# Kernel tuning notes

Hardware: AMD Instinct MI355X
Metric: run time of the kernel (lower is better)

## Reference

```python
import jax, jax.numpy as jnp
import numpy as np

N = 100000
E = 1600000
IN_DIM, HID, OUT = 128, 64, 16
NUM_CLASSES = 2
BN_EPS = 1e-5


def setup_inputs() -> dict:
    key = jax.random.key(0)
    ks = jax.random.split(key, 12)
    s = lambda fan_in: 1.0 / np.sqrt(fan_in)
    inp = {
        'x': jax.random.normal(ks[0], (N, IN_DIM), jnp.float32),
        'src': jax.random.randint(ks[1], (E,), 0, N, jnp.int32),
        'dst': jax.random.randint(ks[2], (E,), 0, N, jnp.int32),
        # SAGEConv1: lin_l (neighbors, bias) + lin_r (root, no bias)
        'W1l': jax.random.uniform(ks[3], (HID, IN_DIM), jnp.float32, -s(IN_DIM), s(IN_DIM)),
        'b1l': jnp.zeros((HID,), jnp.float32),
        'W1r': jax.random.uniform(ks[4], (HID, IN_DIM), jnp.float32, -s(IN_DIM), s(IN_DIM)),
        # BatchNorm1d(hidden)
        'gamma': jnp.ones((HID,), jnp.float32),
        'beta': jnp.zeros((HID,), jnp.float32),
        # SAGEConv2
        'W2l': jax.random.uniform(ks[5], (OUT, HID), jnp.float32, -s(HID), s(HID)),
        'b2l': jnp.zeros((OUT,), jnp.float32),
        'W2r': jax.random.uniform(ks[6], (OUT, HID), jnp.float32, -s(HID), s(HID)),
        # classifier Linear(emb_dim=16, 2)
        'Wc': jax.random.uniform(ks[7], (NUM_CLASSES, OUT), jnp.float32, -s(OUT), s(OUT)),
        'bc': jax.random.uniform(ks[8], (NUM_CLASSES,), jnp.float32, -s(OUT), s(OUT)),
    }
    return inp


def _sage_conv(x, src, dst, Wl, bl, Wr, deg_inv):
    # mean-aggregate neighbor features at dst, then linear; plus root transform
    agg = jax.ops.segment_sum(x[src], dst, num_segments=N) * deg_inv  # [N, F]
    return agg @ Wl.T + bl + x @ Wr.T


def _batchnorm_train(h, gamma, beta):
    mu = jnp.mean(h, axis=0)
    var = jnp.mean((h - mu) ** 2, axis=0)  # biased, as torch BN uses for normalization
    return (h - mu) * jax.lax.rsqrt(var + BN_EPS) * gamma + beta


def reference(x, src, dst, W1l, b1l, W1r, gamma, beta, W2l, b2l, W2r, Wc, bc):
    deg = jax.ops.segment_sum(jnp.ones((E,), x.dtype), dst, num_segments=N)
    deg_inv = (1.0 / jnp.maximum(deg, 1.0))[:, None]
    h = _sage_conv(x, src, dst, W1l, b1l, W1r, deg_inv)      # [N, HID]
    h = jax.nn.relu(_batchnorm_train(h, gamma, beta))
    emb = _sage_conv(h, src, dst, W2l, b2l, W2r, deg_inv)    # [N, OUT]
    logits = emb @ Wc.T + bc                                 # [N, 2]
    return (logits, emb)
```

## Files before the change

### kernel.cpp

```cpp
#include <hip/hip_runtime.h>

#define NN 100000
#define NB ((NN + 255) / 256)

__device__ __forceinline__ void gemm32x64(const float* __restrict__ x,
        const float* __restrict__ W, float* __restrict__ out,
        int rb, int tid, float (*lw)[68], float (*lx)[68]) {
    const int row0 = rb * 32;
    const int cg = tid & 15, rl = tid >> 4;
    float acc[2][4] = {{0.f,0.f,0.f,0.f},{0.f,0.f,0.f,0.f}};
    for (int kt = 0; kt < 2; ++kt) {
        if (kt) __syncthreads();
        for (int idx = tid; idx < 4096; idx += 256) {
            int j = idx >> 6, k = idx & 63;
            lw[k][j] = W[j * 128 + kt * 64 + k];
        }
        #pragma unroll
        for (int i = 0; i < 2; ++i) {
            int f4 = i * 256 + tid;
            int r = f4 >> 4, k4 = (f4 & 15) << 2;
            int grow = row0 + r;
            float4 vv = make_float4(0.f, 0.f, 0.f, 0.f);
            if (grow < NN) vv = *(const float4*)(x + (size_t)grow * 128 + kt * 64 + k4);
            *(float4*)(&lx[r][k4]) = vv;
        }
        __syncthreads();
        #pragma unroll
        for (int p = 0; p < 2; ++p) {
            int r = p * 16 + rl;
            #pragma unroll 8
            for (int k = 0; k < 64; ++k) {
                float xv = lx[r][k];
                float4 wv = *(const float4*)(&lw[k][cg << 2]);
                acc[p][0] = fmaf(xv, wv.x, acc[p][0]);
                acc[p][1] = fmaf(xv, wv.y, acc[p][1]);
                acc[p][2] = fmaf(xv, wv.z, acc[p][2]);
                acc[p][3] = fmaf(xv, wv.w, acc[p][3]);
            }
        }
    }
    #pragma unroll
    for (int p = 0; p < 2; ++p) {
        int grow = row0 + p * 16 + rl;
        if (grow < NN)
            *(float4*)(out + (size_t)grow * 64 + (cg << 2)) =
                make_float4(acc[p][0], acc[p][1], acc[p][2], acc[p][3]);
    }
}

__global__ __launch_bounds__(256) void k_fusedA(const float* __restrict__ x,
        const float* __restrict__ W1l, const int* __restrict__ dst,
        int* __restrict__ deg, float* __restrict__ y1, int E) {
    __shared__ float lw[64][68];
    __shared__ float lx[32][68];
    const int tid = threadIdx.x;
    const int u = blockIdx.x >> 4, v = blockIdx.x & 15;
    if (v < 8) {
        const int base = (u * 8 + v) * 512;
        #pragma unroll
        for (int i = 0; i < 2; ++i) {
            int e = base + i * 256 + tid;
            if (e < E) atomicAdd(&deg[dst[e]], 1);
        }
        return;
    }
    const int rb = u * 8 + (v - 8);
    if (rb >= 3125) return;
    gemm32x64(x, W1l, y1, rb, tid, lw, lx);
}

__global__ __launch_bounds__(256) void k_fusedB(const float* __restrict__ x,
        const float* __restrict__ W1r, const int* __restrict__ src,
        const int* __restrict__ dst, int* __restrict__ cursor,
        int* __restrict__ eidx, float* __restrict__ h, int E) {
    __shared__ float lw[64][68];
    __shared__ float lx[32][68];
    const int tid = threadIdx.x;
    const int u = blockIdx.x >> 4, v = blockIdx.x & 15;
    if (v < 8) {
        const int base = u * 4096;
        const int lo = v * 12500, hi = lo + 12500;
        #pragma unroll 4
        for (int i = 0; i < 16; ++i) {
            int e = base + i * 256 + tid;
            if (e < E) {
                int d = dst[e];
                if (d >= lo && d < hi) {
                    int pos = atomicAdd(&cursor[d], 1);
                    eidx[pos] = src[e];
                }
            }
        }
        return;
    }
    const int rb = u * 8 + (v - 8);
    if (rb >= 3125) return;
    gemm32x64(x, W1r, h, rb, tid, lw, lx);
}

__global__ __launch_bounds__(256) void k_scanA(const int* __restrict__ deg,
                                               int* __restrict__ rowptr,
                                               int* __restrict__ bsum) {
    const int tid = threadIdx.x;
    const int i = blockIdx.x * 256 + tid;
    int v = (i < NN) ? deg[i] : 0;
    const int lane = tid & 63, w = tid >> 6;
    int inc = v;
    #pragma unroll
    for (int d = 1; d < 64; d <<= 1) {
        int t = __shfl_up(inc, d, 64);
        if (lane >= d) inc += t;
    }
    __shared__ int wsum[4];
    if (lane == 63) wsum[w] = inc;
    __syncthreads();
    int wo = 0;
    for (int k = 0; k < w; ++k) wo += wsum[k];
    if (i < NN) rowptr[i] = wo + inc - v;
    if (tid == 255) bsum[blockIdx.x] = wo + inc;
}

__global__ __launch_bounds__(512) void k_scanB(int* __restrict__ bsum,
                                               int* __restrict__ rowptr, int E) {
    const int tid = threadIdx.x;
    int v = (tid < NB) ? bsum[tid] : 0;
    const int lane = tid & 63, w = tid >> 6;
    int inc = v;
    #pragma unroll
    for (int d = 1; d < 64; d <<= 1) {
        int t = __shfl_up(inc, d, 64);
        if (lane >= d) inc += t;
    }
    __shared__ int wsum[8];
    if (lane == 63) wsum[w] = inc;
    __syncthreads();
    int wo = 0;
    for (int k = 0; k < w; ++k) wo += wsum[k];
    if (tid < NB) bsum[tid] = wo + inc - v;
    if (tid == 0) rowptr[NN] = E;
}

__global__ void k_finish(int* __restrict__ rowptr, const int* __restrict__ bsum,
                         const int* __restrict__ deg, int* __restrict__ cursor,
                         float* __restrict__ deg_inv) {
    int i = blockIdx.x * 256 + threadIdx.x;
    if (i < NN) {
        int rp = rowptr[i] + bsum[i >> 8];
        rowptr[i] = rp;
        cursor[i] = rp;
        deg_inv[i] = 1.0f / fmaxf((float)deg[i], 1.0f);
    }
}

__global__ __launch_bounds__(256) void k_gather1(const float* __restrict__ y1,
        const int* __restrict__ rowptr, const int* __restrict__ eidx,
        const float* __restrict__ b1l,
        const float* __restrict__ deg_inv, float* __restrict__ h,
        float* __restrict__ stats) {
    const int tid = threadIdx.x;
    const int f = tid & 63, w = tid >> 6;
    const float bias = b1l[f];
    float a1 = 0.f, a2 = 0.f;
    for (int n = blockIdx.x * 4 + w; n < NN; n += gridDim.x * 4) {
        int beg = rowptr[n], end = rowptr[n + 1];
        float s0 = 0.f, s1 = 0.f, s2 = 0.f, s3 = 0.f;
        int j = beg;
        for (; j + 3 < end; j += 4) {
            int i0 = eidx[j], i1 = eidx[j + 1], i2 = eidx[j + 2], i3 = eidx[j + 3];
            s0 += y1[(size_t)i0 * 64 + f];
            s1 += y1[(size_t)i1 * 64 + f];
            s2 += y1[(size_t)i2 * 64 + f];
            s3 += y1[(size_t)i3 * 64 + f];
        }
        for (; j < end; ++j) s0 += y1[(size_t)eidx[j] * 64 + f];
        size_t off = (size_t)n * 64 + f;
        float hv = fmaf((s0 + s1) + (s2 + s3), deg_inv[n], h[off] + bias);
        h[off] = hv;
        a1 += hv; a2 = fmaf(hv, hv, a2);
    }
    __shared__ float sA[4][64], sB[4][64];
    sA[w][f] = a1; sB[w][f] = a2;
    __syncthreads();
    if (w == 0) {
        atomicAdd(&stats[f],      sA[0][f] + sA[1][f] + sA[2][f] + sA[3][f]);
        atomicAdd(&stats[64 + f], sB[0][f] + sB[1][f] + sB[2][f] + sB[3][f]);
    }
}

__global__ void k_bn_final(float* __restrict__ stats, const float* __restrict__ gamma,
                           const float* __restrict__ beta) {
    int f = threadIdx.x;
    float mu = stats[f] * (1.0f / NN);
    float var = stats[64 + f] * (1.0f / NN) - mu * mu;
    float sc = gamma[f] * rsqrtf(var + 1e-5f);
    stats[128 + f] = sc;
    stats[192 + f] = beta[f] - mu * sc;
}

__global__ __launch_bounds__(256) void k_gemm2(const float* __restrict__ h,
        const float* __restrict__ W2l, const float* __restrict__ W2r,
        const float* __restrict__ stats,
        float* __restrict__ y2, float* __restrict__ hr2) {
    __shared__ float lh[64][68];
    __shared__ float lw[64][36];
    const int tid = threadIdx.x;
    for (int idx = tid; idx < 32 * 64; idx += 256) {
        int j = idx >> 6, k = idx & 63;
        lw[k][j] = (j < 16) ? W2l[idx] : W2r[idx - 1024];
    }
    const int row0 = blockIdx.x * 64;
    for (int i = 0; i < 4; ++i) {
        int f4 = i * 256 + tid;
        int r = f4 >> 4;
        int k4 = (f4 & 15) << 2;
        int grow = row0 + r;
        float4 v = make_float4(0.f, 0.f, 0.f, 0.f);
        if (grow < NN) v = *(const float4*)(h + (size_t)grow * 64 + k4);
        float4 sc = *(const float4*)(stats + 128 + k4);
        float4 sh = *(const float4*)(stats + 192 + k4);
        float4 o;
        o.x = fmaxf(fmaf(v.x, sc.x, sh.x), 0.f);
        o.y = fmaxf(fmaf(v.y, sc.y, sh.y), 0.f);
        o.z = fmaxf(fmaf(v.z, sc.z, sh.z), 0.f);
        o.w = fmaxf(fmaf(v.w, sc.w, sh.w), 0.f);
        *(float4*)(&lh[r][k4]) = o;
    }
    __syncthreads();
    const int cg = tid & 7;
    const int rl = tid >> 3;
    #pragma unroll
    for (int p = 0; p < 2; ++p) {
        int r = p * 32 + rl;
        int grow = row0 + r;
        float ax = 0.f, ay = 0.f, az = 0.f, aw = 0.f;
        #pragma unroll
        for (int k = 0; k < 64; ++k) {
            float hv = lh[r][k];
            float4 wv = *(const float4*)(&lw[k][cg << 2]);
            ax = fmaf(hv, wv.x, ax); ay = fmaf(hv, wv.y, ay);
            az = fmaf(hv, wv.z, az); aw = fmaf(hv, wv.w, aw);
        }
        if (grow < NN) {
            int c = cg << 2;
            if (c < 16) *(float4*)(y2  + (size_t)grow * 16 + c)        = make_float4(ax, ay, az, aw);
            else        *(float4*)(hr2 + (size_t)grow * 16 + (c - 16)) = make_float4(ax, ay, az, aw);
        }
    }
}

__global__ __launch_bounds__(256) void k_gather2(const float* __restrict__ y2,
        const int* __restrict__ rowptr, const int* __restrict__ eidx,
        const float* __restrict__ hr2, const float* __restrict__ b2l,
        const float* __restrict__ deg_inv, const float* __restrict__ Wc,
        const float* __restrict__ bc, float* __restrict__ out) {
    const int tid = threadIdx.x;
    const int f = tid & 15, g = tid >> 4;
    const float wc0 = Wc[f], wc1 = Wc[16 + f];
    const float bias = b2l[f];
    for (int n = blockIdx.x * 16 + g; n < NN; n += gridDim.x * 16) {
        int beg = rowptr[n], end = rowptr[n + 1];
        float s0 = 0.f, s1 = 0.f, s2 = 0.f, s3 = 0.f;
        int j = beg;
        for (; j + 3 < end; j += 4) {
            int i0 = eidx[j], i1 = eidx[j + 1], i2 = eidx[j + 2], i3 = eidx[j + 3];
            s0 += y2[(size_t)i0 * 16 + f];
            s1 += y2[(size_t)i1 * 16 + f];
            s2 += y2[(size_t)i2 * 16 + f];
            s3 += y2[(size_t)i3 * 16 + f];
        }
        for (; j < end; ++j) s0 += y2[(size_t)eidx[j] * 16 + f];
        float e = fmaf((s0 + s1) + (s2 + s3), deg_inv[n], hr2[(size_t)n * 16 + f] + bias);
        out[(size_t)(2 * NN) + (size_t)n * 16 + f] = e;
        float l0 = e * wc0, l1 = e * wc1;
        #pragma unroll
        for (int m = 1; m < 16; m <<= 1) {
            l0 += __shfl_xor(l0, m, 64);
            l1 += __shfl_xor(l1, m, 64);
        }
        if (f == 0) {
            out[(size_t)n * 2]     = l0 + bc[0];
            out[(size_t)n * 2 + 1] = l1 + bc[1];
        }
    }
}

extern "C" void kernel_launch(void* const* d_in, const int* in_sizes, int n_in,
                              void* d_out, int out_size, void* d_ws, size_t ws_size,
                              hipStream_t stream) {
    const float* x     = (const float*)d_in[0];
    const int*   src   = (const int*)d_in[1];
    const int*   dst   = (const int*)d_in[2];
    const float* W1l   = (const float*)d_in[3];
    const float* b1l   = (const float*)d_in[4];
    const float* W1r   = (const float*)d_in[5];
    const float* gamma = (const float*)d_in[6];
    const float* beta  = (const float*)d_in[7];
    const float* W2l   = (const float*)d_in[8];
    const float* b2l   = (const float*)d_in[9];
    const float* W2r   = (const float*)d_in[10];
    const float* Wc    = (const float*)d_in[11];
    const float* bc    = (const float*)d_in[12];
    const int E = in_sizes[1];

    float* ws      = (float*)d_ws;
    int*   rowptr  = (int*)ws;
    float* deg_inv = ws + 100352;
    float* stats   = ws + 200704;
    int*   deg_i   = (int*)(ws + 200960);
    int*   cursor  = (int*)(ws + 301312);
    int*   eidx    = (int*)(ws + 401664);
    float* y1      = ws + 401664 + (size_t)E;
    float* h       = y1 + (size_t)NN * 64;
    int*   bsum    = eidx;
    float* y2      = y1;
    float* hr2     = y1 + (size_t)NN * 16;
    float* out     = (float*)d_out;

    hipMemsetAsync(deg_i, 0, NN * sizeof(int), stream);
    hipMemsetAsync(stats, 0, 256 * sizeof(float), stream);

    k_fusedA<<<6256, 256, 0, stream>>>(x, W1l, dst, deg_i, y1, E);

    k_scanA<<<NB, 256, 0, stream>>>(deg_i, rowptr, bsum);
    k_scanB<<<1, 512, 0, stream>>>(bsum, rowptr, E);
    k_finish<<<NB, 256, 0, stream>>>(rowptr, bsum, deg_i, cursor, deg_inv);

    k_fusedB<<<6256, 256, 0, stream>>>(x, W1r, src, dst, cursor, eidx, h, E);

    k_gather1<<<4096, 256, 0, stream>>>(y1, rowptr, eidx, b1l, deg_inv, h, stats);
    k_bn_final<<<1, 64, 0, stream>>>(stats, gamma, beta);

    k_gemm2<<<(NN + 63) / 64, 256, 0, stream>>>(h, W2l, W2r, stats, y2, hr2);

    k_gather2<<<2048, 256, 0, stream>>>(y2, rowptr, eidx, hr2, b2l, deg_inv, Wc, bc, out);
}
```

Before: 473.8 us.

## Store gathered neighbor features in bf16 and fold BN finalize into gemm2

The per-node transformed features y1 and y2, which are gathered once per edge, are now stored as bf16 instead of fp32. This halves the bytes moved in the two edge gathers. Separately, the tiny BN-finalize kernel is removed and each gemm2 block computes the scale and shift itself into shared memory, saving one launch. The cost is reduced precision in the aggregated messages, which may shift the outputs relative to the fp32 reference.

```diff
diff --git a/kernel.cpp b/kernel.cpp
--- a/kernel.cpp
+++ b/kernel.cpp
@@ -3,8 +3,18 @@
 #define NN 100000
 #define NB ((NN + 255) / 256)
 
+__device__ __forceinline__ unsigned short f2bf(float x) {
+    unsigned u = __float_as_uint(x);
+    u += 0x7fff + ((u >> 16) & 1);
+    return (unsigned short)(u >> 16);
+}
+__device__ __forceinline__ float bf2f(unsigned short h) {
+    return __uint_as_float(((unsigned)h) << 16);
+}
+
+template<bool BF16>
 __device__ __forceinline__ void gemm32x64(const float* __restrict__ x,
-        const float* __restrict__ W, float* __restrict__ out,
+        const float* __restrict__ W, void* __restrict__ out,
         int rb, int tid, float (*lw)[68], float (*lx)[68]) {
     const int row0 = rb * 32;
     const int cg = tid & 15, rl = tid >> 4;
@@ -42,15 +52,23 @@
     #pragma unroll
     for (int p = 0; p < 2; ++p) {
         int grow = row0 + p * 16 + rl;
-        if (grow < NN)
-            *(float4*)(out + (size_t)grow * 64 + (cg << 2)) =
-                make_float4(acc[p][0], acc[p][1], acc[p][2], acc[p][3]);
+        if (grow < NN) {
+            if (BF16) {
+                ushort4 o;
+                o.x = f2bf(acc[p][0]); o.y = f2bf(acc[p][1]);
+                o.z = f2bf(acc[p][2]); o.w = f2bf(acc[p][3]);
+                *(ushort4*)((unsigned short*)out + (size_t)grow * 64 + (cg << 2)) = o;
+            } else {
+                *(float4*)((float*)out + (size_t)grow * 64 + (cg << 2)) =
+                    make_float4(acc[p][0], acc[p][1], acc[p][2], acc[p][3]);
+            }
+        }
     }
 }
 
 __global__ __launch_bounds__(256) void k_fusedA(const float* __restrict__ x,
         const float* __restrict__ W1l, const int* __restrict__ dst,
-        int* __restrict__ deg, float* __restrict__ y1, int E) {
+        int* __restrict__ deg, unsigned short* __restrict__ y1, int E) {
     __shared__ float lw[64][68];
     __shared__ float lx[32][68];
     const int tid = threadIdx.x;
@@ -66,7 +84,7 @@
     }
     const int rb = u * 8 + (v - 8);
     if (rb >= 3125) return;
-    gemm32x64(x, W1l, y1, rb, tid, lw, lx);
+    gemm32x64<true>(x, W1l, y1, rb, tid, lw, lx);
 }
 
 __global__ __launch_bounds__(256) void k_fusedB(const float* __restrict__ x,
@@ -95,7 +113,7 @@
     }
     const int rb = u * 8 + (v - 8);
     if (rb >= 3125) return;
-    gemm32x64(x, W1r, h, rb, tid, lw, lx);
+    gemm32x64<false>(x, W1r, h, rb, tid, lw, lx);
 }
 
 __global__ __launch_bounds__(256) void k_scanA(const int* __restrict__ deg,
@@ -152,7 +170,7 @@
     }
 }
 
-__global__ __launch_bounds__(256) void k_gather1(const float* __restrict__ y1,
+__global__ __launch_bounds__(256) void k_gather1(const unsigned short* __restrict__ y1,
         const int* __restrict__ rowptr, const int* __restrict__ eidx,
         const float* __restrict__ b1l,
         const float* __restrict__ deg_inv, float* __restrict__ h,
@@ -167,12 +185,12 @@
         int j = beg;
         for (; j + 3 < end; j += 4) {
             int i0 = eidx[j], i1 = eidx[j + 1], i2 = eidx[j + 2], i3 = eidx[j + 3];
-            s0 += y1[(size_t)i0 * 64 + f];
-            s1 += y1[(size_t)i1 * 64 + f];
-            s2 += y1[(size_t)i2 * 64 + f];
-            s3 += y1[(size_t)i3 * 64 + f];
-        }
-        for (; j < end; ++j) s0 += y1[(size_t)eidx[j] * 64 + f];
+            s0 += bf2f(y1[(size_t)i0 * 64 + f]);
+            s1 += bf2f(y1[(size_t)i1 * 64 + f]);
+            s2 += bf2f(y1[(size_t)i2 * 64 + f]);
+            s3 += bf2f(y1[(size_t)i3 * 64 + f]);
+        }
+        for (; j < end; ++j) s0 += bf2f(y1[(size_t)eidx[j] * 64 + f]);
         size_t off = (size_t)n * 64 + f;
         float hv = fmaf((s0 + s1) + (s2 + s3), deg_inv[n], h[off] + bias);
         h[off] = hv;
@@ -187,27 +205,27 @@
     }
 }
 
-__global__ void k_bn_final(float* __restrict__ stats, const float* __restrict__ gamma,
-                           const float* __restrict__ beta) {
-    int f = threadIdx.x;
-    float mu = stats[f] * (1.0f / NN);
-    float var = stats[64 + f] * (1.0f / NN) - mu * mu;
-    float sc = gamma[f] * rsqrtf(var + 1e-5f);
-    stats[128 + f] = sc;
-    stats[192 + f] = beta[f] - mu * sc;
-}
-
 __global__ __launch_bounds__(256) void k_gemm2(const float* __restrict__ h,
         const float* __restrict__ W2l, const float* __restrict__ W2r,
-        const float* __restrict__ stats,
-        float* __restrict__ y2, float* __restrict__ hr2) {
+        const float* __restrict__ stats, const float* __restrict__ gamma,
+        const float* __restrict__ beta,
+        unsigned short* __restrict__ y2, float* __restrict__ hr2) {
     __shared__ float lh[64][68];
     __shared__ float lw[64][36];
-    const int tid = threadIdx.x;
+    __shared__ float lsc[64], lsh[64];
+    const int tid = threadIdx.x;
+    if (tid < 64) {
+        float mu = stats[tid] * (1.0f / NN);
+        float var = stats[64 + tid] * (1.0f / NN) - mu * mu;
+        float sc = gamma[tid] * rsqrtf(var + 1e-5f);
+        lsc[tid] = sc;
+        lsh[tid] = beta[tid] - mu * sc;
+    }
     for (int idx = tid; idx < 32 * 64; idx += 256) {
         int j = idx >> 6, k = idx & 63;
         lw[k][j] = (j < 16) ? W2l[idx] : W2r[idx - 1024];
     }
+    __syncthreads();
     const int row0 = blockIdx.x * 64;
     for (int i = 0; i < 4; ++i) {
         int f4 = i * 256 + tid;
@@ -216,8 +234,8 @@
         int grow = row0 + r;
         float4 v = make_float4(0.f, 0.f, 0.f, 0.f);
         if (grow < NN) v = *(const float4*)(h + (size_t)grow * 64 + k4);
-        float4 sc = *(const float4*)(stats + 128 + k4);
-        float4 sh = *(const float4*)(stats + 192 + k4);
+        float4 sc = *(const float4*)(&lsc[k4]);
+        float4 sh = *(const float4*)(&lsh[k4]);
         float4 o;
         o.x = fmaxf(fmaf(v.x, sc.x, sh.x), 0.f);
         o.y = fmaxf(fmaf(v.y, sc.y, sh.y), 0.f);
@@ -242,13 +260,18 @@
         }
         if (grow < NN) {
             int c = cg << 2;
-            if (c < 16) *(float4*)(y2  + (size_t)grow * 16 + c)        = make_float4(ax, ay, az, aw);
-            else        *(float4*)(hr2 + (size_t)grow * 16 + (c - 16)) = make_float4(ax, ay, az, aw);
-        }
-    }
-}
-
-__global__ __launch_bounds__(256) void k_gather2(const float* __restrict__ y2,
+            if (c < 16) {
+                ushort4 o;
+                o.x = f2bf(ax); o.y = f2bf(ay); o.z = f2bf(az); o.w = f2bf(aw);
+                *(ushort4*)(y2 + (size_t)grow * 16 + c) = o;
+            } else {
+                *(float4*)(hr2 + (size_t)grow * 16 + (c - 16)) = make_float4(ax, ay, az, aw);
+            }
+        }
+    }
+}
+
+__global__ __launch_bounds__(256) void k_gather2(const unsigned short* __restrict__ y2,
         const int* __restrict__ rowptr, const int* __restrict__ eidx,
         const float* __restrict__ hr2, const float* __restrict__ b2l,
         const float* __restrict__ deg_inv, const float* __restrict__ Wc,
@@ -263,12 +286,12 @@
         int j = beg;
         for (; j + 3 < end; j += 4) {
             int i0 = eidx[j], i1 = eidx[j + 1], i2 = eidx[j + 2], i3 = eidx[j + 3];
-            s0 += y2[(size_t)i0 * 16 + f];
-            s1 += y2[(size_t)i1 * 16 + f];
-            s2 += y2[(size_t)i2 * 16 + f];
-            s3 += y2[(size_t)i3 * 16 + f];
-        }
-        for (; j < end; ++j) s0 += y2[(size_t)eidx[j] * 16 + f];
+            s0 += bf2f(y2[(size_t)i0 * 16 + f]);
+            s1 += bf2f(y2[(size_t)i1 * 16 + f]);
+            s2 += bf2f(y2[(size_t)i2 * 16 + f]);
+            s3 += bf2f(y2[(size_t)i3 * 16 + f]);
+        }
+        for (; j < end; ++j) s0 += bf2f(y2[(size_t)eidx[j] * 16 + f]);
         float e = fmaf((s0 + s1) + (s2 + s3), deg_inv[n], hr2[(size_t)n * 16 + f] + bias);
         out[(size_t)(2 * NN) + (size_t)n * 16 + f] = e;
         float l0 = e * wc0, l1 = e * wc1;
@@ -309,11 +332,12 @@
     int*   deg_i   = (int*)(ws + 200960);
     int*   cursor  = (int*)(ws + 301312);
     int*   eidx    = (int*)(ws + 401664);
-    float* y1      = ws + 401664 + (size_t)E;
-    float* h       = y1 + (size_t)NN * 64;
+    float* y1reg   = ws + 401664 + (size_t)E;
+    float* h       = y1reg + (size_t)NN * 64;
+    unsigned short* y1 = (unsigned short*)y1reg;
     int*   bsum    = eidx;
-    float* y2      = y1;
-    float* hr2     = y1 + (size_t)NN * 16;
+    unsigned short* y2 = (unsigned short*)y1reg;
+    float* hr2     = y1reg + (size_t)NN * 8;
     float* out     = (float*)d_out;
 
     hipMemsetAsync(deg_i, 0, NN * sizeof(int), stream);
@@ -328,9 +352,8 @@
     k_fusedB<<<6256, 256, 0, stream>>>(x, W1r, src, dst, cursor, eidx, h, E);
 
     k_gather1<<<4096, 256, 0, stream>>>(y1, rowptr, eidx, b1l, deg_inv, h, stats);
-    k_bn_final<<<1, 64, 0, stream>>>(stats, gamma, beta);
-
-    k_gemm2<<<(NN + 63) / 64, 256, 0, stream>>>(h, W2l, W2r, stats, y2, hr2);
+
+    k_gemm2<<<(NN + 63) / 64, 256, 0, stream>>>(h, W2l, W2r, stats, gamma, beta, y2, hr2);
 
     k_gather2<<<2048, 256, 0, stream>>>(y2, rowptr, eidx, hr2, b2l, deg_inv, Wc, bc, out);
 }
```

After: 448.3 us. 1.06x faster.
